# Kernel tuning notes

Measured on AMD Instinct MI355X. Metric: run time of the kernel, lower is better.

## Reference

```python
import jax, jax.numpy as jnp
import numpy as np

CUTOFF = 5.0          # module init kwarg
N_BASIS = 64
PI_HALF = np.pi / 2.0  # self.pi_half buffer, the C parameter in the formula


def setup_inputs() -> dict:
    key = jax.random.key(0)
    k1, k2 = jax.random.split(key)
    N, box = 2048, 10.0
    # per-point scalar feature (density-like, positive)
    f = jax.random.uniform(k1, (N, 1), dtype=jnp.float32)
    # 3D coordinates in a box; cutoff=5.0 so the Step mask is nontrivial
    coords = jax.random.uniform(k2, (N, 3), dtype=jnp.float32) * box
    # buffers from __init__: means = linspace(0, cutoff, n_basis) / cutoff, beta = (scale*n_basis)^2
    means = jnp.linspace(0.0, CUTOFF, N_BASIS, dtype=jnp.float32) / CUTOFF
    beta = jnp.asarray(float(N_BASIS) ** 2, dtype=jnp.float32)
    return {"f": f, "coords": coords, "means": means, "beta": beta}


def reference(f, coords, means, beta):
    # forward: coords (and out_coords==coords) are divided by cutoff, so all
    # distances below are in normalized units and the cutoff is at d == 1.
    c = coords / CUTOFF                      # [N, 3]
    diff = c[:, None, :] - c[None, :, :]     # [N, M, 3]  (R_i - r_j)
    sq = jnp.sum(diff * diff, axis=-1)       # [N, M]
    d = jnp.sqrt(jnp.maximum(sq, 1e-12))     # Norm2(R - r), safe at d=0
    # Cos(C*d) * Step(1 - d) * F_j   -> scalar pair weight [N, M]
    w = jnp.cos(PI_HALF * d) * (d <= 1.0).astype(f.dtype) * f[:, 0][None, :]
    # Exp(-B * (d - M_b)^2)          -> Gaussian basis expansion [N, M, n_basis]
    g = jnp.exp(-beta * (d[..., None] - means) ** 2)
    # Sum reduction over j (axis=1 in Genred)
    return jnp.einsum('nm,nmb->nb', w, g)    # [N, n_basis]
```

## Files before the change

kernel.cpp:

```cpp
#include <hip/hip_runtime.h>
#include <math.h>

#define NB 64
#define BLOCK 256
#define WPB 4
#define KHALF 48
#define NA 112
#define GUARD 3
#define QLEN 70
#define WSTRIDE (16 * QLEN)
#define WTOT (2 * WSTRIDE)

#define S0F   1048576.0f
#define S1R   6710886.4f
#define S1DEC 33554432.0f

#if __has_builtin(__builtin_amdgcn_exp2f)
#define EXP2F(x) __builtin_amdgcn_exp2f(x)
#else
#define EXP2F(x) exp2f(x)
#endif
#if __has_builtin(__builtin_amdgcn_cosf)
#define COSREV(x) __builtin_amdgcn_cosf(x)
#else
#define COSREV(x) __cosf(6.28318530718f * (x))
#endif
#if __has_builtin(__builtin_amdgcn_sqrtf)
#define SQRTF(x) __builtin_amdgcn_sqrtf(x)
#else
#define SQRTF(x) sqrtf(x)
#endif

__global__ void __launch_bounds__(BLOCK, 8)
wgp_kernel(const float* __restrict__ f,
           const float* __restrict__ coords,
           const float* __restrict__ means,
           const float* __restrict__ beta,
           float* __restrict__ out,
           int n_pts) {
    __shared__ int    W[WTOT];
    __shared__ float2 A[NA];
    __shared__ float  red[WPB][NB];

    const int tid  = threadIdx.x;
    const int lane = tid & 63;
    const int wid  = tid >> 6;
    const int n    = blockIdx.x;

    int4* W4 = (int4*)W;
#pragma unroll
    for (int i = tid; i < WTOT / 4; i += BLOCK) W4[i] = make_int4(0, 0, 0, 0);

    const float h      = 1.0f / 1008.0f;
    const float hr     = 5.0f / 1008.0f;
    const float beta_v = beta[0];
    const float kk     = -1.44269504089f * beta_v;

    if (tid < NA) {
        const int   k = tid - KHALF;
        const float u = (float)k * h;
        const float E = (k <= KHALF) ? EXP2F(kk * u * u) : 0.0f;
        const float h2_12 = h * h * (1.0f / 12.0f);
        const float corr  = 1.0f + (2.0f * beta_v * beta_v * u * u - beta_v) * h2_12;
        A[tid] = make_float2(E * corr * (1.0f / S0F),
                             (-2.0f * beta_v * u * E) * (1.0f / S1DEC));
    }

    const float xn = coords[3 * n + 0];
    const float yn = coords[3 * n + 1];
    const float zn = coords[3 * n + 2];

    __syncthreads();

    const int chunks = (n_pts + BLOCK - 1) / BLOCK;
#pragma unroll 4
    for (int c = 0; c < chunks; ++c) {
        const int m = c * BLOCK + tid;
        if (m < n_pts) {
            const float px = coords[3 * m + 0];
            const float py = coords[3 * m + 1];
            const float pz = coords[3 * m + 2];
            const float fm = f[m];
            const float dx = xn - px;
            const float dy = yn - py;
            const float dz = zn - pz;
            const float sqr = fmaf(dx, dx, fmaf(dy, dy, dz * dz));
            if (sqr <= 25.0f) {
                const float s  = SQRTF(sqr);
                const float w  = COSREV(0.05f * s) * fm;
                const int   j  = (int)fmaf(s, 201.6f, 0.5f);
                const float dl = fmaf((float)j, -hr, s);
                const int off  = (j & 15) * QLEN + (j >> 4) + GUARD;
                atomicAdd(&W[off],           (int)(w * S0F));
                atomicAdd(&W[WSTRIDE + off], (int)(w * dl * S1R));
            }
        }
    }
    __syncthreads();

    float acc = 0.f;
    {
        const int r0 = 4 * wid;
        int p0[7], p1[7], q0[7], q1[7];

#define LOADW(B0, B1, RHO) do {                              \
            const int base_ = (RHO) * QLEN + lane;           \
            _Pragma("unroll")                                \
            for (int t = 0; t < 7; ++t) {                    \
                B0[t] = W[base_ + t];                        \
                B1[t] = W[WSTRIDE + base_ + t];              \
            }                                                \
        } while (0)

#define FMAS(B0, B1, RHO) do {                               \
            _Pragma("unroll")                                \
            for (int t = 0; t < 7; ++t) {                    \
                const float2 a_ = A[16 * t + (RHO)];         \
                acc = fmaf(a_.x, (float)B0[t], acc);         \
                acc = fmaf(a_.y, (float)B1[t], acc);         \
            }                                                \
        } while (0)

        LOADW(p0, p1, r0);
        LOADW(q0, q1, r0 + 1);
        FMAS(p0, p1, r0);
        LOADW(p0, p1, r0 + 2);
        FMAS(q0, q1, r0 + 1);
        LOADW(q0, q1, r0 + 3);
        FMAS(p0, p1, r0 + 2);
        FMAS(q0, q1, r0 + 3);

#undef LOADW
#undef FMAS
    }

    red[wid][lane] = acc;
    __syncthreads();
    if (wid == 0) {
        out[n * NB + lane] = (red[0][lane] + red[1][lane])
                           + (red[2][lane] + red[3][lane]);
    }
}

extern "C" void kernel_launch(void* const* d_in, const int* in_sizes, int n_in,
                              void* d_out, int out_size, void* d_ws, size_t ws_size,
                              hipStream_t stream) {
    const float* f      = (const float*)d_in[0];
    const float* coords = (const float*)d_in[1];
    const float* means  = (const float*)d_in[2];
    const float* beta   = (const float*)d_in[3];
    float* out = (float*)d_out;

    const int n = in_sizes[0];
    wgp_kernel<<<n, BLOCK, 0, stream>>>(f, coords, means, beta, out, n);
}
```

Before: 65.63 us.

## Pack paired fixed-point accumulators into one 64-bit LDS atomic and readlane coefficients

Replaces the two separate 32-bit LDS atomics per neighbour with a single 64-bit atomic add on a packed word: the low half holds the value accumulator and the high half holds the slope accumulator, with the carry from the low half relying on the unsigned interpretation. Gaussian coefficient tables move out of shared memory into per-lane registers and are broadcast with readlane during the reduction, which removes the A array and its LDS reads. The aim is to halve the atomic traffic and cut LDS usage. The risk is low-half overflow or carry into the high half, which would corrupt the slope sums if the fixed-point sums ever go negative or large.

```diff
diff --git a/kernel.cpp b/kernel.cpp
--- a/kernel.cpp
+++ b/kernel.cpp
@@ -5,11 +5,9 @@
 #define BLOCK 256
 #define WPB 4
 #define KHALF 48
-#define NA 112
 #define GUARD 3
 #define QLEN 70
-#define WSTRIDE (16 * QLEN)
-#define WTOT (2 * WSTRIDE)
+#define NW64 (16 * QLEN)
 
 #define S0F   1048576.0f
 #define S1R   6710886.4f
@@ -31,6 +29,12 @@
 #define SQRTF(x) sqrtf(x)
 #endif
 
+#if __has_builtin(__builtin_amdgcn_readlane)
+#define RDLANE(v, l) __builtin_amdgcn_readlane((v), (l))
+#else
+#define RDLANE(v, l) __shfl((v), (l), 64)
+#endif
+
 __global__ void __launch_bounds__(BLOCK, 8)
 wgp_kernel(const float* __restrict__ f,
            const float* __restrict__ coords,
@@ -38,37 +42,42 @@
            const float* __restrict__ beta,
            float* __restrict__ out,
            int n_pts) {
-    __shared__ int    W[WTOT];
-    __shared__ float2 A[NA];
-    __shared__ float  red[WPB][NB];
+    __shared__ unsigned long long W64[NW64];
+    __shared__ float red[WPB][NB];
 
     const int tid  = threadIdx.x;
     const int lane = tid & 63;
     const int wid  = tid >> 6;
     const int n    = blockIdx.x;
 
-    int4* W4 = (int4*)W;
+    int4* W4 = (int4*)W64;
 #pragma unroll
-    for (int i = tid; i < WTOT / 4; i += BLOCK) W4[i] = make_int4(0, 0, 0, 0);
+    for (int i = tid; i < NW64 / 2; i += BLOCK) W4[i] = make_int4(0, 0, 0, 0);
 
     const float h      = 1.0f / 1008.0f;
     const float hr     = 5.0f / 1008.0f;
     const float beta_v = beta[0];
     const float kk     = -1.44269504089f * beta_v;
 
-    if (tid < NA) {
-        const int   k = tid - KHALF;
-        const float u = (float)k * h;
-        const float E = (k <= KHALF) ? EXP2F(kk * u * u) : 0.0f;
-        const float h2_12 = h * h * (1.0f / 12.0f);
-        const float corr  = 1.0f + (2.0f * beta_v * beta_v * u * u - beta_v) * h2_12;
-        A[tid] = make_float2(E * corr * (1.0f / S0F),
-                             (-2.0f * beta_v * u * E) * (1.0f / S1DEC));
-    }
-
     const float xn = coords[3 * n + 0];
     const float yn = coords[3 * n + 1];
     const float zn = coords[3 * n + 2];
+
+    float a0v = 0.0f, a1v = 0.0f;
+    {
+        const int t  = lane >> 2;
+        const int rr = lane & 3;
+        const int kidx = 16 * t + 4 * wid + rr;
+        const int k    = kidx - KHALF;
+        if (lane < 28) {
+            const float u = (float)k * h;
+            const float E = (k <= KHALF) ? EXP2F(kk * u * u) : 0.0f;
+            const float h2_12 = h * h * (1.0f / 12.0f);
+            const float corr  = 1.0f + (2.0f * beta_v * beta_v * u * u - beta_v) * h2_12;
+            a0v = E * corr * (1.0f / S0F);
+            a1v = (-2.0f * beta_v * u * E) * (1.0f / S1DEC);
+        }
+    }
 
     __syncthreads();
 
@@ -91,8 +100,12 @@
                 const int   j  = (int)fmaf(s, 201.6f, 0.5f);
                 const float dl = fmaf((float)j, -hr, s);
                 const int off  = (j & 15) * QLEN + (j >> 4) + GUARD;
-                atomicAdd(&W[off],           (int)(w * S0F));
-                atomicAdd(&W[WSTRIDE + off], (int)(w * dl * S1R));
+                const int w0i  = (int)(w * S0F);
+                const int w1i  = (int)(w * dl * S1R);
+                const unsigned long long inc =
+                    (((unsigned long long)(long long)w1i) << 32)
+                    + (unsigned long long)(unsigned)w0i;
+                atomicAdd(&W64[off], inc);
             }
         }
     }
@@ -100,38 +113,40 @@
 
     float acc = 0.f;
     {
+        const int2* Wv = (const int2*)W64;
         const int r0 = 4 * wid;
-        int p0[7], p1[7], q0[7], q1[7];
+        int2 p[7], q[7];
 
-#define LOADW(B0, B1, RHO) do {                              \
+#define SA0(T, RR) __int_as_float(RDLANE(__float_as_int(a0v), 4 * (T) + (RR)))
+#define SA1(T, RR) __int_as_float(RDLANE(__float_as_int(a1v), 4 * (T) + (RR)))
+
+#define LOADW(B, RHO) do {                                   \
             const int base_ = (RHO) * QLEN + lane;           \
             _Pragma("unroll")                                \
+            for (int t = 0; t < 7; ++t) B[t] = Wv[base_ + t];\
+        } while (0)
+
+#define FMAS(B, RR) do {                                     \
+            _Pragma("unroll")                                \
             for (int t = 0; t < 7; ++t) {                    \
-                B0[t] = W[base_ + t];                        \
-                B1[t] = W[WSTRIDE + base_ + t];              \
+                acc = fmaf(SA0(t, RR), (float)(unsigned)B[t].x, acc); \
+                acc = fmaf(SA1(t, RR), (float)B[t].y, acc);  \
             }                                                \
         } while (0)
 
-#define FMAS(B0, B1, RHO) do {                               \
-            _Pragma("unroll")                                \
-            for (int t = 0; t < 7; ++t) {                    \
-                const float2 a_ = A[16 * t + (RHO)];         \
-                acc = fmaf(a_.x, (float)B0[t], acc);         \
-                acc = fmaf(a_.y, (float)B1[t], acc);         \
-            }                                                \
-        } while (0)
-
-        LOADW(p0, p1, r0);
-        LOADW(q0, q1, r0 + 1);
-        FMAS(p0, p1, r0);
-        LOADW(p0, p1, r0 + 2);
-        FMAS(q0, q1, r0 + 1);
-        LOADW(q0, q1, r0 + 3);
-        FMAS(p0, p1, r0 + 2);
-        FMAS(q0, q1, r0 + 3);
+        LOADW(p, r0);
+        LOADW(q, r0 + 1);
+        FMAS(p, 0);
+        LOADW(p, r0 + 2);
+        FMAS(q, 1);
+        LOADW(q, r0 + 3);
+        FMAS(p, 2);
+        FMAS(q, 3);
 
 #undef LOADW
 #undef FMAS
+#undef SA0
+#undef SA1
     }
 
     red[wid][lane] = acc;
```

Measured after the change: 65.69 us. Within noise of the previous version (+0.1%).
